# Performance work log

Hardware: AMD Instinct MI355X
Metric: run time of the kernel (lower is better)

The kernel has to match this reference:

```python
import jax, jax.numpy as jnp
import numpy as np

N, D_IN, H, D_OUT = 32, 1024, 2048, 256
P = H * D_IN + H + D_OUT * H + D_OUT  # flattened params per network
SCALE = 4e-4  # ~1/sqrt(2P): keeps pairwise ||diff||^2 = O(1) so exp(-d/2) doesn't underflow
EPS = 0.1     # step size used in optimize()


def setup_inputs() -> dict:
    key = jax.random.key(0)
    k1, k2, k3, k4, k5, k6 = jax.random.split(key, 6)
    return {
        "W1": jax.random.normal(k1, (N, H, D_IN), jnp.float32) * SCALE,
        "b1": jax.random.normal(k2, (N, H), jnp.float32) * SCALE,
        "W2": jax.random.normal(k3, (N, D_OUT, H), jnp.float32) * SCALE,
        "b2": jax.random.normal(k4, (N, D_OUT), jnp.float32) * SCALE,
        "X": jax.random.normal(k5, (4096, D_IN), jnp.float32),
        "y": jax.random.normal(k6, (4096, D_OUT), jnp.float32),
    }


def reference(W1, b1, W2, b2, X, y):
    # One SVGD iteration (do_one_iteration with eps=0.1), vectorized over the
    # ensemble. Faithful to the source's actual math:
    #   dlogp_i = d/dz log_prior + d/dz log_prior = -2*theta_i   (likelihood grad
    #   is computed but discarded in derivative_log_posterior_compute, so X, y
    #   do not affect the update)
    #   kd(i,j) = exp(-||theta_i - theta_j||^2 / 2),  dkd_i = -kd*(theta_i-theta_j)
    #   phi_i = (1/n) * sum_{j=1..n-1} [ kd(i,j)*dlogp_i + dkd(i,j) ]
    #         = (1/n) * ( -3*S_i*theta_i + sum_{j>=1} kd(i,j)*theta_j ),  S_i = sum_{j>=1} kd(i,j)
    #   theta_i <- theta_i + eps*phi_i
    n = W1.shape[0]
    theta = jnp.concatenate(
        [W1.reshape(n, -1), b1, W2.reshape(n, -1), b2], axis=1
    )  # [n, P]
    sq = jnp.sum(theta * theta, axis=1)                      # [n]
    d2 = sq[:, None] + sq[None, :] - 2.0 * (theta @ theta.T)  # [n, n] squared dists
    K = jnp.exp(-0.5 * jnp.maximum(d2, 0.0))                  # RBF kernel, sigma=1
    Kj = K[:, 1:]                                             # loop runs j = 1..n-1
    S = jnp.sum(Kj, axis=1)                                   # [n]
    phi = (-3.0 * S[:, None] * theta + Kj @ theta[1:]) / n    # [n, P]
    return theta + EPS * phi
```

## Files before the change

kernel.cpp:

```cpp
#include <hip/hip_runtime.h>
#include <hip/hip_bf16.h>
#include <stdint.h>

#define NP     32
#define P_W1   2097152
#define P_B1   2048
#define P_W2   524288
#define P_B2   256
#define OFFB1  2097152
#define OFFW2  2099200
#define OFFB2  2623488
#define P_TOT  2623744
#define EPS_F  0.1f
#define NCHUNK (P_TOT / 256)

typedef short  bf16x8 __attribute__((ext_vector_type(8)));
typedef float  f32x16 __attribute__((ext_vector_type(16)));

__device__ __forceinline__ short f2bf(float x) {
    uint32_t u = __builtin_bit_cast(uint32_t, x);
    u += 0x7fffu + ((u >> 16) & 1u);
    return (short)(u >> 16);
}

struct Seg { const float* p; int stride; int off; };

__device__ __forceinline__ Seg seg_of(const float* W1, const float* b1,
                                      const float* W2, const float* b2, int pbase) {
    Seg s;
    if (pbase < OFFB1)      { s.p = W1; s.stride = P_W1; s.off = pbase; }
    else if (pbase < OFFW2) { s.p = b1; s.stride = P_B1; s.off = pbase - OFFB1; }
    else if (pbase < OFFB2) { s.p = W2; s.stride = P_W2; s.off = pbase - OFFW2; }
    else                    { s.p = b2; s.stride = P_B2; s.off = pbase - OFFB2; }
    return s;
}

__global__ void zero_kernel(float* __restrict__ G) {
    G[threadIdx.x] = 0.0f;
}

__global__ void __launch_bounds__(256)
gram_kernel(const float* __restrict__ W1, const float* __restrict__ b1,
            const float* __restrict__ W2, const float* __restrict__ b2,
            float* __restrict__ G) {
    const int lane   = threadIdx.x & 63;
    const int wave   = (blockIdx.x * 256 + threadIdx.x) >> 6;
    const int nwaves = gridDim.x * 4;
    const int row    = lane & 31;
    const int q      = lane >> 5;

    f32x16 acc;
    #pragma unroll
    for (int r = 0; r < 16; r++) acc[r] = 0.0f;

    for (int c = wave; c < P_TOT / 64; c += nwaves) {
        const int kb = c * 64;
        Seg s = seg_of(W1, b1, W2, b2, kb);
        const float* base = s.p + (size_t)row * s.stride + s.off + q * 8;

        #pragma unroll
        for (int cc = 0; cc < 4; cc++) {
            const float4 lo = *reinterpret_cast<const float4*>(base + cc * 16);
            const float4 hi = *reinterpret_cast<const float4*>(base + cc * 16 + 4);
            bf16x8 f;
            f[0] = f2bf(lo.x); f[1] = f2bf(lo.y); f[2] = f2bf(lo.z); f[3] = f2bf(lo.w);
            f[4] = f2bf(hi.x); f[5] = f2bf(hi.y); f[6] = f2bf(hi.z); f[7] = f2bf(hi.w);
            acc = __builtin_amdgcn_mfma_f32_32x32x16_bf16(f, f, acc, 0, 0, 0);
        }
    }

    #pragma unroll
    for (int r = 0; r < 16; r++) {
        const int orow = (r & 3) + 8 * (r >> 2) + 4 * q;
        atomicAdd(&G[orow * 32 + row], acc[r]);
    }
}

__global__ void computeM_kernel(const float* __restrict__ G, float* __restrict__ Mp) {
    __shared__ float Ks[32][32];
    const int t = threadIdx.x;
    const int i = t >> 5, j = t & 31;
    const float sqi = G[i * 33];
    const float sqj = G[j * 33];
    const float d2  = fmaxf(sqi + sqj - 2.0f * G[i * 32 + j], 0.0f);
    const float K   = expf(-0.5f * d2);
    Ks[i][j] = K;
    __syncthreads();
    float S = 0.0f;
    for (int m = 1; m < 32; m++) S += Ks[i][m];
    float v = (j >= 1) ? (EPS_F / 32.0f) * K : 0.0f;
    if (i == j) v += 1.0f - (3.0f * EPS_F / 32.0f) * S;
    Mp[i * 32 + j] = v;
}

__global__ void __launch_bounds__(256)
apply_kernel(const float* __restrict__ W1, const float* __restrict__ b1,
             const float* __restrict__ W2, const float* __restrict__ b2,
             const float* __restrict__ Mp, float* __restrict__ out) {
    const int lane   = threadIdx.x & 63;
    const int wave   = (blockIdx.x * 256 + threadIdx.x) >> 6;
    const int nwaves = gridDim.x * 4;

    for (int ch = wave; ch < NCHUNK; ch += nwaves) {
        const int pbase = ch * 256;
        Seg s = seg_of(W1, b1, W2, b2, pbase);
        const float* sp = s.p + s.off + lane * 4;
        const size_t str = (size_t)s.stride;

        float4 th[32];
        #pragma unroll
        for (int j = 0; j < 32; ++j)
            th[j] = *reinterpret_cast<const float4*>(sp + j * str);

        float* op = out + (size_t)pbase + lane * 4;
        #pragma unroll 1
        for (int i = 0; i < 32; ++i) {
            const float* mrow = Mp + i * 32;
            float ax = 0.f, ay = 0.f, az = 0.f, aw = 0.f;
            #pragma unroll
            for (int j = 0; j < 32; ++j) {
                const float m = mrow[j];
                ax = fmaf(m, th[j].x, ax);
                ay = fmaf(m, th[j].y, ay);
                az = fmaf(m, th[j].z, az);
                aw = fmaf(m, th[j].w, aw);
            }
            float4 o = { ax, ay, az, aw };
            *reinterpret_cast<float4*>(op + (size_t)i * P_TOT) = o;
        }
    }
}

extern "C" void kernel_launch(void* const* d_in, const int* in_sizes, int n_in,
                              void* d_out, int out_size, void* d_ws, size_t ws_size,
                              hipStream_t stream) {
    const float* W1 = (const float*)d_in[0];
    const float* b1 = (const float*)d_in[1];
    const float* W2 = (const float*)d_in[2];
    const float* b2 = (const float*)d_in[3];
    float* out = (float*)d_out;
    float* G   = (float*)d_ws;
    float* Mp  = G + 1024;

    zero_kernel<<<1, 1024, 0, stream>>>(G);
    gram_kernel<<<2048, 256, 0, stream>>>(W1, b1, W2, b2, G);
    computeM_kernel<<<1, 1024, 0, stream>>>(G, Mp);
    apply_kernel<<<1024, 256, 0, stream>>>(W1, b1, W2, b2, Mp, out);
}
```

Measured before the change: 804.5 us.

## Stage gram tiles through LDS with coalesced loads, prefetch, and block-level reduction

```diff
diff --git a/kernel.cpp b/kernel.cpp
--- a/kernel.cpp
+++ b/kernel.cpp
@@ -43,36 +43,65 @@
 gram_kernel(const float* __restrict__ W1, const float* __restrict__ b1,
             const float* __restrict__ W2, const float* __restrict__ b2,
             float* __restrict__ G) {
-    const int lane   = threadIdx.x & 63;
-    const int wave   = (blockIdx.x * 256 + threadIdx.x) >> 6;
-    const int nwaves = gridDim.x * 4;
-    const int row    = lane & 31;
-    const int q      = lane >> 5;
+    __shared__ __align__(16) unsigned char smem[16384];
+    const int tid  = threadIdx.x;
+    const int lane = tid & 63;
+    const int w    = tid >> 6;
+    const int r31  = lane & 31;
+    const int q    = lane >> 5;
 
     f32x16 acc;
     #pragma unroll
     for (int r = 0; r < 16; r++) acc[r] = 0.0f;
 
-    for (int c = wave; c < P_TOT / 64; c += nwaves) {
-        const int kb = c * 64;
-        Seg s = seg_of(W1, b1, W2, b2, kb);
-        const float* base = s.p + (size_t)row * s.stride + s.off + q * 8;
+    float4 cur[8];
+    auto issue = [&](int c) {
+        Seg s = seg_of(W1, b1, W2, b2, c * 256);
+        #pragma unroll
+        for (int j = 0; j < 8; j++) {
+            const int row = 8 * w + j;
+            cur[j] = *reinterpret_cast<const float4*>(
+                s.p + (size_t)row * s.stride + s.off + lane * 4);
+        }
+    };
 
+    int c = blockIdx.x;
+    if (c < NCHUNK) issue(c);
+    for (; c < NCHUNK; c += gridDim.x) {
+        #pragma unroll
+        for (int j = 0; j < 8; j++) {
+            const int row = 8 * w + j;
+            uint32_t lo = ((uint32_t)(uint16_t)f2bf(cur[j].y) << 16) | (uint16_t)f2bf(cur[j].x);
+            uint32_t hi = ((uint32_t)(uint16_t)f2bf(cur[j].w) << 16) | (uint16_t)f2bf(cur[j].z);
+            uint2 pk = { lo, hi };
+            const int boff = row * 512 + ((lane * 8) ^ (j << 4));
+            *reinterpret_cast<uint2*>(smem + boff) = pk;
+        }
+        __syncthreads();
+        const int cn = c + (int)gridDim.x;
+        if (cn < NCHUNK) issue(cn);
         #pragma unroll
         for (int cc = 0; cc < 4; cc++) {
-            const float4 lo = *reinterpret_cast<const float4*>(base + cc * 16);
-            const float4 hi = *reinterpret_cast<const float4*>(base + cc * 16 + 4);
-            bf16x8 f;
-            f[0] = f2bf(lo.x); f[1] = f2bf(lo.y); f[2] = f2bf(lo.z); f[3] = f2bf(lo.w);
-            f[4] = f2bf(hi.x); f[5] = f2bf(hi.y); f[6] = f2bf(hi.z); f[7] = f2bf(hi.w);
+            const int colb = w * 128 + cc * 32 + q * 16;
+            const int boff = r31 * 512 + (colb ^ ((r31 & 7) << 4));
+            bf16x8 f = *reinterpret_cast<const bf16x8*>(smem + boff);
             acc = __builtin_amdgcn_mfma_f32_32x32x16_bf16(f, f, acc, 0, 0, 0);
         }
+        __syncthreads();
     }
 
+    float* red = reinterpret_cast<float*>(smem);
     #pragma unroll
     for (int r = 0; r < 16; r++) {
         const int orow = (r & 3) + 8 * (r >> 2) + 4 * q;
-        atomicAdd(&G[orow * 32 + row], acc[r]);
+        red[w * 1024 + orow * 32 + r31] = acc[r];
+    }
+    __syncthreads();
+    #pragma unroll
+    for (int e = 0; e < 4; e++) {
+        const int idx = tid * 4 + e;
+        const float v = red[idx] + red[1024 + idx] + red[2048 + idx] + red[3072 + idx];
+        atomicAdd(&G[idx], v);
     }
 }
 
@@ -143,7 +172,7 @@
     float* Mp  = G + 1024;
 
     zero_kernel<<<1, 1024, 0, stream>>>(G);
-    gram_kernel<<<2048, 256, 0, stream>>>(W1, b1, W2, b2, G);
+    gram_kernel<<<1024, 256, 0, stream>>>(W1, b1, W2, b2, G);
     computeM_kernel<<<1, 1024, 0, stream>>>(G, Mp);
     apply_kernel<<<1024, 256, 0, stream>>>(W1, b1, W2, b2, Mp, out);
 }
```

Measured after the change: 744.7 us. 7.4% less time.
